# Kernel tuning notes

Hardware: AMD Instinct MI355X
Metric: run time of the kernel (lower is better)

Reference implementation:

```python
import jax, jax.numpy as jnp
import numpy as np

D_MODEL = 1024
N_HEAD = 16
HEAD_DIM = D_MODEL // N_HEAD
N_POS = 4096
K_PROJ = 256  # self.k is hardcoded to 256 in the module
BATCH = 4


def setup_inputs() -> dict:
    key = jax.random.key(0)
    ks = jax.random.split(key, 11)
    s = 1.0 / np.sqrt(D_MODEL)
    return {
        "x": jax.random.normal(ks[0], (BATCH, N_POS, D_MODEL), jnp.float32),
        "Wq": jax.random.normal(ks[1], (D_MODEL, D_MODEL), jnp.float32) * s,
        "bq": jnp.zeros((D_MODEL,), jnp.float32),
        "Wk": jax.random.normal(ks[2], (D_MODEL, D_MODEL), jnp.float32) * s,
        "bk": jnp.zeros((D_MODEL,), jnp.float32),
        "Wv": jax.random.normal(ks[3], (D_MODEL, D_MODEL), jnp.float32) * s,
        "bv": jnp.zeros((D_MODEL,), jnp.float32),
        "E": jax.random.normal(ks[4], (K_PROJ, N_POS), jnp.float32),
        "F": jax.random.normal(ks[5], (K_PROJ, N_POS), jnp.float32),
        "Wo": jax.random.normal(ks[6], (D_MODEL, D_MODEL), jnp.float32) * s,
        "bo": jnp.zeros((D_MODEL,), jnp.float32),
    }


def reference(x, Wq, bq, Wk, bk, Wv, bv, E, F, Wo, bo):
    B, N, D = x.shape
    scale = jnp.sqrt(jnp.asarray(HEAD_DIM, x.dtype))
    # Q/K/V projections (nn.Linear applies x @ W.T + b)
    def proj(W, b):
        y = jnp.einsum('bnd,ed->bne', x, W) + b
        return y.reshape(B, N, N_HEAD, HEAD_DIM).transpose(0, 2, 1, 3)  # bhnd
    Q = proj(Wq, bq)
    K = proj(Wk, bk)
    V = proj(Wv, bv)
    # Linformer low-rank projections along sequence dim
    Kp = jnp.einsum('kn,bhnd->bhkd', E, K)
    Vp = jnp.einsum('kn,bhnd->bhkd', F, V)
    attn_score = jnp.einsum('bhnd,bhkd->bhnk', Q, Kp) / scale
    attn = jax.nn.softmax(attn_score, axis=-1)  # dropout is identity (drop_prob=0)
    out = jnp.einsum('bhnk,bhkd->bhnd', attn, Vp)
    out = out.transpose(0, 2, 1, 3).reshape(B, N, D)
    out = jnp.einsum('bnd,ed->bne', out, Wo) + bo
    return out, attn_score
```

## Files before the change

kernel.cpp:

```cpp
#include <hip/hip_runtime.h>

typedef _Float16 f16;
typedef __attribute__((ext_vector_type(8))) _Float16 f16x8;
typedef __attribute__((ext_vector_type(4))) _Float16 f16x4;
typedef __attribute__((ext_vector_type(4))) float f32x4;

typedef const __attribute__((address_space(1))) unsigned int* gas_ptr;
typedef __attribute__((address_space(3))) unsigned int* las_ptr;

__device__ __forceinline__ void gload16(const f16* g, f16* l) {
  __builtin_amdgcn_global_load_lds((gas_ptr)g, (las_ptr)l, 16, 0, 0);
}

template<int WM, int WN, bool OUT32>
__device__ __forceinline__ void gemm_core(
    const f16* __restrict__ A, int lda,
    const f16* __restrict__ B, int ldb,
    int kLen,
    f16* lsA, f16* lsB,
    float* __restrict__ C32, f16* __restrict__ C16, int ldc,
    float scale, const float* __restrict__ biasC, const float* __restrict__ biasR)
{
  constexpr int T   = WM * WN * 64;
  constexpr int nA  = (WM * 64 * 8) / T;
  constexpr int nB  = (WN * 64 * 8) / T;
  constexpr int RPI = T / 8;
  const int t    = threadIdx.x;
  const int lane = t & 63;
  const int wave = t >> 6;
  const int wm   = wave / WN;
  const int wn   = wave % WN;

  f32x4 acc[4][4];
  const f32x4 z4 = {0.f, 0.f, 0.f, 0.f};
#pragma unroll
  for (int i = 0; i < 4; ++i)
#pragma unroll
    for (int j = 0; j < 4; ++j) acc[i][j] = z4;

  const int r_ = t >> 3;
  const int c_ = (t & 7) * 8;
  const int ldsOff = (wave << 9);

  for (int kt = 0; kt < kLen; kt += 64) {
#pragma unroll
    for (int i = 0; i < nA; ++i) {
      const f16* g = A + (size_t)(i * RPI + r_) * lda + kt + c_;
      gload16(g, lsA + i * (T * 8) + ldsOff);
    }
#pragma unroll
    for (int i = 0; i < nB; ++i) {
      const f16* g = B + (size_t)(i * RPI + r_) * ldb + kt + c_;
      gload16(g, lsB + i * (T * 8) + ldsOff);
    }
    __syncthreads();
#pragma unroll
    for (int ks = 0; ks < 2; ++ks) {
      f16x8 af[4], bf[4];
#pragma unroll
      for (int i = 0; i < 4; ++i)
        af[i] = *(const f16x8*)&lsA[(wm * 64 + i * 16 + (lane & 15)) * 64 + ks * 32 + (lane >> 4) * 8];
#pragma unroll
      for (int j = 0; j < 4; ++j)
        bf[j] = *(const f16x8*)&lsB[(wn * 64 + j * 16 + (lane & 15)) * 64 + ks * 32 + (lane >> 4) * 8];
#pragma unroll
      for (int i = 0; i < 4; ++i)
#pragma unroll
        for (int j = 0; j < 4; ++j)
          acc[i][j] = __builtin_amdgcn_mfma_f32_16x16x32_f16(af[i], bf[j], acc[i][j], 0, 0, 0);
    }
    __syncthreads();
  }

  const int lc = lane & 15;
  const int lr = (lane >> 4) * 4;
#pragma unroll
  for (int j = 0; j < 4; ++j) {
    const int col = wn * 64 + j * 16 + lc;
    const float bC = biasC ? biasC[col] : 0.f;
#pragma unroll
    for (int i = 0; i < 4; ++i) {
      const int rbase = wm * 64 + i * 16 + lr;
#pragma unroll
      for (int r = 0; r < 4; ++r) {
        const int row = rbase + r;
        float v = acc[i][j][r] * scale + bC;
        if (biasR) v += biasR[row];
        if (OUT32) C32[(size_t)row * ldc + col] = v;
        else       C16[(size_t)row * ldc + col] = (f16)v;
      }
    }
  }
}

template<int WM, int WN, bool OUT32>
__global__ __launch_bounds__(WM * WN * 64) void k_gemm(
    const f16* A, int lda, const f16* B, int ldb, int kLen,
    float* C32, f16* C16, int ldc, float scale,
    const float* biasC, const float* biasR)
{
  __shared__ f16 lsA[WM * 64 * 64];
  __shared__ f16 lsB[WN * 64 * 64];
  const size_t rt = blockIdx.y, ct = blockIdx.x;
  gemm_core<WM, WN, OUT32>(
      A + rt * (WM * 64) * (size_t)lda, lda,
      B + ct * (WN * 64) * (size_t)ldb, ldb, kLen,
      lsA, lsB,
      OUT32 ? C32 + rt * (WM * 64) * (size_t)ldc + ct * (WN * 64) : nullptr,
      OUT32 ? nullptr : C16 + rt * (WM * 64) * (size_t)ldc + ct * (WN * 64), ldc,
      scale,
      biasC ? biasC + ct * (WN * 64) : nullptr,
      biasR ? biasR + rt * (WM * 64) : nullptr);
}

__global__ __launch_bounds__(256) void k_cast_xt(const float* __restrict__ x,
                                                 f16* __restrict__ Xf,
                                                 f16* __restrict__ XT)
{
  __shared__ f16 tile[64][68];
  const int b = blockIdx.z, bi = blockIdx.y, bj = blockIdx.x;
  const int r0 = threadIdx.x >> 4;
  const int c4 = (threadIdx.x & 15) * 4;
  const float* xb = x + ((size_t)b * 4096 + (size_t)bi * 64) * 1024 + bj * 64;
#pragma unroll
  for (int rr = 0; rr < 4; ++rr) {
    const int row = rr * 16 + r0;
    const float4 v = *(const float4*)(xb + (size_t)row * 1024 + c4);
    f16x4 h = {(f16)v.x, (f16)v.y, (f16)v.z, (f16)v.w};
    *(f16x4*)&tile[row][c4] = h;
    *(f16x4*)(Xf + ((size_t)b * 4096 + (size_t)bi * 64 + row) * 1024 + bj * 64 + c4) = h;
  }
  __syncthreads();
#pragma unroll
  for (int rr = 0; rr < 4; ++rr) {
    const int col = rr * 16 + r0;
    f16x4 h = {tile[c4 + 0][col], tile[c4 + 1][col], tile[c4 + 2][col], tile[c4 + 3][col]};
    *(f16x4*)(XT + ((size_t)b * 1024 + (size_t)bj * 64 + col) * 4096 + (size_t)bi * 64 + c4) = h;
  }
}

__global__ __launch_bounds__(256) void k_cast_w(
    const float* w0, const float* w1, const float* w2,
    const float* w3, const float* w4, const float* w5, f16* __restrict__ d)
{
  const size_t i = ((size_t)blockIdx.x * 256 + threadIdx.x) * 4;
  const int seg = (int)(i >> 20);
  const float* s = (seg == 0) ? w0 : (seg == 1) ? w1 : (seg == 2) ? w2
                 : (seg == 3) ? w3 : (seg == 4) ? w4 : w5;
  const float4 v = *(const float4*)(s + (i & 1048575));
  f16x4 o = {(f16)v.x, (f16)v.y, (f16)v.z, (f16)v.w};
  *(f16x4*)(d + i) = o;
}

__global__ __launch_bounds__(256) void k_rowsum(const float* __restrict__ E,
                                                const float* __restrict__ F,
                                                float* __restrict__ rs)
{
  const int r = blockIdx.x * 4 + (threadIdx.x >> 6);
  const int lane = threadIdx.x & 63;
  const float* src = (r < 256) ? (E + (size_t)r * 4096) : (F + (size_t)(r - 256) * 4096);
  float s = 0.f;
#pragma unroll
  for (int i = 0; i < 16; ++i) {
    const float4 v = *(const float4*)(src + i * 256 + lane * 4);
    s += v.x + v.y + v.z + v.w;
  }
#pragma unroll
  for (int o = 32; o; o >>= 1) s += __shfl_xor(s, o);
  if (lane == 0) rs[r] = s;
}

__global__ __launch_bounds__(256) void k_exfx(const f16* __restrict__ EF,
                                              const f16* __restrict__ XT,
                                              float* __restrict__ part)
{
  __shared__ f16 lsA[128 * 64];
  __shared__ f16 lsB[128 * 64];
  const int z = blockIdx.z; const int b = z & 3; const int s = z >> 2;
  const int rt = blockIdx.y, ct = blockIdx.x;
  const f16* A = EF + (size_t)rt * 128 * 4096 + s * 1024;
  const f16* B = XT + (size_t)b * 1024 * 4096 + (size_t)ct * 128 * 4096 + s * 1024;
  float* C = part + (size_t)z * (512 * 1024) + (size_t)rt * 128 * 1024 + ct * 128;
  gemm_core<2, 2, true>(A, 4096, B, 4096, 1024, lsA, lsB, C, nullptr, 1024, 1.f, nullptr, nullptr);
}

__global__ __launch_bounds__(256) void k_reduce2(const float* __restrict__ part,
                                                 f16* __restrict__ EXf)
{
  const size_t i = ((size_t)blockIdx.x * 256 + threadIdx.x) * 4;
  const size_t b = i >> 19;
  const size_t idx = i & 524287;
  const float4 a = *(const float4*)(part + (0 * 4 + b) * 524288 + idx);
  const float4 c1 = *(const float4*)(part + (1 * 4 + b) * 524288 + idx);
  const float4 c2 = *(const float4*)(part + (2 * 4 + b) * 524288 + idx);
  const float4 c3 = *(const float4*)(part + (3 * 4 + b) * 524288 + idx);
  f16x4 o = {(f16)(a.x + c1.x + c2.x + c3.x), (f16)(a.y + c1.y + c2.y + c3.y),
             (f16)(a.z + c1.z + c2.z + c3.z), (f16)(a.w + c1.w + c2.w + c3.w)};
  *(f16x4*)(EXf + i) = o;
}

__global__ __launch_bounds__(256) void k_kpvp(const f16* __restrict__ EXf,
                                              const f16* __restrict__ W16,
                                              float* __restrict__ p2)
{
  __shared__ f16 lsA[128 * 64];
  __shared__ f16 lsB[128 * 64];
  const int z = blockIdx.z; const int which = z & 1; const int s = z >> 1;
  const int rt = blockIdx.y, ct = blockIdx.x;
  const f16 *A, *B;
  if (which == 0) {
    const int b = rt >> 1, r0 = (rt & 1) * 128;
    A = EXf + ((size_t)b * 512 + r0) * 1024 + s * 512;
    B = W16 + 1048576 + (size_t)ct * 128 * 1024 + s * 512;
  } else {
    const int b = ct >> 1, r0 = (ct & 1) * 128;
    A = W16 + 2 * 1048576 + (size_t)rt * 128 * 1024 + s * 512;
    B = EXf + ((size_t)b * 512 + 256 + r0) * 1024 + s * 512;
  }
  float* C = p2 + (size_t)(s * 2 + which) * 1048576 + (size_t)rt * 128 * 1024 + ct * 128;
  gemm_core<2, 2, true>(A, 1024, B, 1024, 512, lsA, lsB, C, nullptr, 1024, 1.f, nullptr, nullptr);
}

__global__ __launch_bounds__(256) void k_reduce3(const float* __restrict__ p2,
                                                 f16* __restrict__ KpVp,
                                                 const float* __restrict__ rs,
                                                 const float* __restrict__ bk,
                                                 const float* __restrict__ bv)
{
  const size_t i = ((size_t)blockIdx.x * 256 + threadIdx.x) * 4;
  const int half = (int)(i >> 20);
  const size_t j = i & 1048575;
  size_t pidx; float r1[4];
  if (half == 0) {
    const int r  = (int)((j >> 10) & 255);
    const int hd = (int)(j & 1023);
    pidx = j;
    const float se = rs[r];
#pragma unroll
    for (int t = 0; t < 4; ++t) r1[t] = se * bk[hd + t];
  } else {
    const int b  = (int)(j >> 18);
    const int hd = (int)((j >> 8) & 1023);
    const int r  = (int)(j & 255);
    pidx = (size_t)hd * 1024 + (size_t)b * 256 + r;
    const float bb = bv[hd];
#pragma unroll
    for (int t = 0; t < 4; ++t) r1[t] = bb * rs[256 + r + t];
  }
  const float4 a = *(const float4*)(p2 + (size_t)(0 * 2 + half) * 1048576 + pidx);
  const float4 c = *(const float4*)(p2 + (size_t)(1 * 2 + half) * 1048576 + pidx);
  f16x4 o = {(f16)(a.x + c.x + r1[0]), (f16)(a.y + c.y + r1[1]),
             (f16)(a.z + c.z + r1[2]), (f16)(a.w + c.w + r1[3])};
  *(f16x4*)(KpVp + i) = o;
}

__global__ __launch_bounds__(256) void k_scores(const f16* __restrict__ Q,
                                                const f16* __restrict__ Kp,
                                                float* __restrict__ S)
{
  __shared__ f16 lsA[128 * 64];
  __shared__ f16 lsB[128 * 64];
  const int bh = blockIdx.z; const int b = bh >> 4; const int h = bh & 15;
  const size_t rt = blockIdx.y, ct = blockIdx.x;
  const f16* A = Q + (size_t)b * 4096 * 1024 + h * 64 + rt * 128 * 1024;
  const f16* B = Kp + (size_t)b * 262144 + h * 64 + ct * 128 * 1024;
  float* C = S + (size_t)bh * 4096 * 256 + rt * 128 * 256 + ct * 128;
  gemm_core<2, 2, true>(A, 1024, B, 1024, 64, lsA, lsB, C, nullptr, 256, 0.125f, nullptr, nullptr);
}

__global__ __launch_bounds__(256) void k_pvsm(const float* __restrict__ S,
                                              const f16* __restrict__ VpT,
                                              f16* __restrict__ OP)
{
  __shared__ f16 lsP[128 * 256];
  __shared__ f16 lsV[64 * 256];
  const int rt = blockIdx.x, h = blockIdx.y, b = blockIdx.z;
  const int t = threadIdx.x, lane = t & 63, w = t >> 6;

  const char* Vb = (const char*)(VpT + ((size_t)b * 1024 + h * 64) * 256);
  {
    const int vrow = lane >> 5;
    const int voff = (lane & 31) * 16;
#pragma unroll
    for (int i = 0; i < 8; ++i) {
      const int row = i * 8 + w * 2 + vrow;
      const int so = voff ^ ((row & 7) << 4);
      gload16((const f16*)(Vb + (size_t)row * 512 + so),
              (f16*)((char*)lsV + i * 4096 + w * 1024));
    }
  }

  const float* Sb = S + (((size_t)(b * 16 + h)) * 4096 + (size_t)rt * 128) * 256;
  const int rg = t >> 4;
  const int li = t & 15;
#pragma unroll
  for (int it = 0; it < 8; ++it) {
    const int row = it * 16 + rg;
    const float* sr = Sb + (size_t)row * 256 + li * 16;
    const float4 v0 = *(const float4*)(sr + 0);
    const float4 v1 = *(const float4*)(sr + 4);
    const float4 v2 = *(const float4*)(sr + 8);
    const float4 v3 = *(const float4*)(sr + 12);
    float m = fmaxf(fmaxf(fmaxf(v0.x, v0.y), fmaxf(v0.z, v0.w)),
                    fmaxf(fmaxf(v1.x, v1.y), fmaxf(v1.z, v1.w)));
    m = fmaxf(m, fmaxf(fmaxf(fmaxf(v2.x, v2.y), fmaxf(v2.z, v2.w)),
                       fmaxf(fmaxf(v3.x, v3.y), fmaxf(v3.z, v3.w))));
#pragma unroll
    for (int o = 8; o; o >>= 1) m = fmaxf(m, __shfl_xor(m, o));
    float ev[16];
    ev[0]  = __expf(v0.x - m); ev[1]  = __expf(v0.y - m);
    ev[2]  = __expf(v0.z - m); ev[3]  = __expf(v0.w - m);
    ev[4]  = __expf(v1.x - m); ev[5]  = __expf(v1.y - m);
    ev[6]  = __expf(v1.z - m); ev[7]  = __expf(v1.w - m);
    ev[8]  = __expf(v2.x - m); ev[9]  = __expf(v2.y - m);
    ev[10] = __expf(v2.z - m); ev[11] = __expf(v2.w - m);
    ev[12] = __expf(v3.x - m); ev[13] = __expf(v3.y - m);
    ev[14] = __expf(v3.z - m); ev[15] = __expf(v3.w - m);
    float s = 0.f;
#pragma unroll
    for (int k2 = 0; k2 < 16; ++k2) s += ev[k2];
#pragma unroll
    for (int o = 8; o; o >>= 1) s += __shfl_xor(s, o);
    const float inv = 1.f / s;
    f16x8 h0, h1;
#pragma unroll
    for (int k2 = 0; k2 < 8; ++k2) {
      h0[k2] = (f16)(ev[k2] * inv);
      h1[k2] = (f16)(ev[8 + k2] * inv);
    }
    char* base = (char*)lsP + (size_t)row * 512;
    const int swz = (row & 7) << 4;
    *(f16x8*)(base + ((li * 32) ^ swz))      = h0;
    *(f16x8*)(base + ((li * 32 + 16) ^ swz)) = h1;
  }
  __syncthreads();

  const int wm = w >> 1, wn = w & 1;
  f32x4 acc[4][2];
  const f32x4 z4 = {0.f, 0.f, 0.f, 0.f};
#pragma unroll
  for (int i = 0; i < 4; ++i) { acc[i][0] = z4; acc[i][1] = z4; }
#pragma unroll
  for (int ks = 0; ks < 8; ++ks) {
    const int koff = ks * 64 + (lane >> 4) * 16;
    f16x8 af[4], bf[2];
#pragma unroll
    for (int i = 0; i < 4; ++i) {
      const int m = wm * 64 + i * 16 + (lane & 15);
      af[i] = *(const f16x8*)((const char*)lsP + (size_t)m * 512 + (koff ^ ((m & 7) << 4)));
    }
#pragma unroll
    for (int j = 0; j < 2; ++j) {
      const int n = wn * 32 + j * 16 + (lane & 15);
      bf[j] = *(const f16x8*)((const char*)lsV + (size_t)n * 512 + (koff ^ ((n & 7) << 4)));
    }
#pragma unroll
    for (int i = 0; i < 4; ++i)
#pragma unroll
      for (int j = 0; j < 2; ++j)
        acc[i][j] = __builtin_amdgcn_mfma_f32_16x16x32_f16(af[i], bf[j], acc[i][j], 0, 0, 0);
  }

  f16* Ob = OP + ((size_t)b * 4096 + (size_t)rt * 128) * 1024 + h * 64;
  const int lc = lane & 15, lr = (lane >> 4) * 4;
#pragma unroll
  for (int j = 0; j < 2; ++j) {
    const int col = wn * 32 + j * 16 + lc;
#pragma unroll
    for (int i = 0; i < 4; ++i) {
      const int rbase = wm * 64 + i * 16 + lr;
#pragma unroll
      for (int r = 0; r < 4; ++r)
        Ob[(size_t)(rbase + r) * 1024 + col] = (f16)acc[i][j][r];
    }
  }
}

extern "C" void kernel_launch(void* const* d_in, const int* in_sizes, int n_in,
                              void* d_out, int out_size, void* d_ws, size_t ws_size,
                              hipStream_t stream) {
  const float* x  = (const float*)d_in[0];
  const float* Wq = (const float*)d_in[1];
  const float* bq = (const float*)d_in[2];
  const float* Wk = (const float*)d_in[3];
  const float* bk = (const float*)d_in[4];
  const float* Wv = (const float*)d_in[5];
  const float* bv = (const float*)d_in[6];
  const float* E  = (const float*)d_in[7];
  const float* F  = (const float*)d_in[8];
  const float* Wo = (const float*)d_in[9];
  const float* bo = (const float*)d_in[10];

  float* out = (float*)d_out;
  float* S   = out + 16777216;

  char* w = (char*)d_ws;
  f16*   Xf     = (f16*)w;
  f16*   EXf    = (f16*)w;
  float* rowsum = (float*)(w + 4 * 1048576);
  f16*   XT     = (f16*)(w + 33554432);
  f16*   OPf    = (f16*)(w + 33554432);
  f16*   Qf     = (f16*)(w + (size_t)2 * 33554432);
  float* part   = (float*)(w + (size_t)3 * 33554432);
  float* part2  = (float*)(w + (size_t)3 * 33554432);
  f16*   W16    = (f16*)(w + (size_t)4 * 33554432);
  f16*   EF16   = W16 + (size_t)4 * 1048576;
  f16*   KpVp   = (f16*)(w + (size_t)4 * 33554432 + 12582912);

  k_cast_xt<<<dim3(16, 64, 4), 256, 0, stream>>>(x, Xf, XT);
  k_cast_w<<<6144, 256, 0, stream>>>(Wq, Wk, Wv, Wo, E, F, W16);

  k_gemm<2, 2, false><<<dim3(8, 128), 256, 0, stream>>>(
      Xf, 1024, W16, 1024, 1024, nullptr, Qf, 1024, 1.f, bq, nullptr);

  k_rowsum<<<128, 256, 0, stream>>>(E, F, rowsum);

  k_exfx<<<dim3(8, 4, 16), 256, 0, stream>>>(EF16, XT, part);
  k_reduce2<<<2048, 256, 0, stream>>>(part, EXf);

  k_kpvp<<<dim3(8, 8, 4), 256, 0, stream>>>(EXf, W16, part2);
  k_reduce3<<<2048, 256, 0, stream>>>(part2, KpVp, rowsum, bk, bv);

  k_scores<<<dim3(2, 32, 64), 256, 0, stream>>>(Qf, KpVp, S);

  k_pvsm<<<dim3(32, 16, 4), 256, 0, stream>>>(S, KpVp + (size_t)4 * 262144, OPf);

  k_gemm<2, 2, true><<<dim3(8, 128), 256, 0, stream>>>(
      OPf, 1024, W16 + 3 * 1048576, 1024, 1024, out, nullptr, 1024, 1.f, bo, nullptr);
}
```

Measured before the change: 724.4 us.

## Fuse score GEMM, softmax and PV GEMM into a single attention kernel

Merges the separate scores kernel and the softmax+PV kernel into one kernel. Each block computes Q·Kp^T for 128 rows in registers, writes the scaled scores to S (still a required output), runs the softmax on the register tiles and stages fp16 probabilities in LDS for the PV MFMA. This removes the global re-read of the 64 MB fp32 score tensor and one kernel launch. In exchange it uses 96 KB of shared memory and large accumulator arrays per thread, which may lower occupancy.

Measured after the change: 654.2 us. 9.7% less time.

```diff
diff --git a/kernel.cpp b/kernel.cpp
--- a/kernel.cpp
+++ b/kernel.cpp
@@ -254,31 +254,36 @@
   *(f16x4*)(KpVp + i) = o;
 }
 
-__global__ __launch_bounds__(256) void k_scores(const f16* __restrict__ Q,
-                                                const f16* __restrict__ Kp,
-                                                float* __restrict__ S)
-{
-  __shared__ f16 lsA[128 * 64];
-  __shared__ f16 lsB[128 * 64];
-  const int bh = blockIdx.z; const int b = bh >> 4; const int h = bh & 15;
-  const size_t rt = blockIdx.y, ct = blockIdx.x;
-  const f16* A = Q + (size_t)b * 4096 * 1024 + h * 64 + rt * 128 * 1024;
-  const f16* B = Kp + (size_t)b * 262144 + h * 64 + ct * 128 * 1024;
-  float* C = S + (size_t)bh * 4096 * 256 + rt * 128 * 256 + ct * 128;
-  gemm_core<2, 2, true>(A, 1024, B, 1024, 64, lsA, lsB, C, nullptr, 256, 0.125f, nullptr, nullptr);
-}
-
-__global__ __launch_bounds__(256) void k_pvsm(const float* __restrict__ S,
+__global__ __launch_bounds__(256) void k_attn(const f16* __restrict__ Q,
+                                              const f16* __restrict__ Kp,
                                               const f16* __restrict__ VpT,
+                                              float* __restrict__ S,
                                               f16* __restrict__ OP)
 {
-  __shared__ f16 lsP[128 * 256];
-  __shared__ f16 lsV[64 * 256];
+  __shared__ char smem[98304];
+  f16* lsK = (f16*)smem;
+  f16* lsQ = (f16*)(smem + 32768);
+  f16* lsV = (f16*)(smem + 65536);
+
   const int rt = blockIdx.x, h = blockIdx.y, b = blockIdx.z;
   const int t = threadIdx.x, lane = t & 63, w = t >> 6;
-
-  const char* Vb = (const char*)(VpT + ((size_t)b * 1024 + h * 64) * 256);
+  const int g = lane >> 4;
+  const int c = lane & 15;
+
+  const int r_ = t >> 3;
+  const int cswz = ((t & 7) * 16) ^ ((r_ & 7) << 4);
+  const char* Kg = (const char*)(Kp + (size_t)b * 262144 + h * 64);
+  const char* Qg = (const char*)(Q + ((size_t)b * 4096 + (size_t)rt * 128) * 1024 + h * 64);
+#pragma unroll
+  for (int i = 0; i < 8; ++i)
+    gload16((const f16*)(Kg + (size_t)(i * 32 + r_) * 2048 + cswz),
+            lsK + i * 2048 + (w << 9));
+#pragma unroll
+  for (int i = 0; i < 4; ++i)
+    gload16((const f16*)(Qg + (size_t)(i * 32 + r_) * 2048 + cswz),
+            lsQ + i * 2048 + (w << 9));
   {
+    const char* Vb = (const char*)(VpT + ((size_t)b * 1024 + h * 64) * 256);
     const int vrow = lane >> 5;
     const int voff = (lane & 31) * 16;
 #pragma unroll
@@ -289,89 +294,110 @@
               (f16*)((char*)lsV + i * 4096 + w * 1024));
     }
   }
-
-  const float* Sb = S + (((size_t)(b * 16 + h)) * 4096 + (size_t)rt * 128) * 256;
-  const int rg = t >> 4;
-  const int li = t & 15;
-#pragma unroll
-  for (int it = 0; it < 8; ++it) {
-    const int row = it * 16 + rg;
-    const float* sr = Sb + (size_t)row * 256 + li * 16;
-    const float4 v0 = *(const float4*)(sr + 0);
-    const float4 v1 = *(const float4*)(sr + 4);
-    const float4 v2 = *(const float4*)(sr + 8);
-    const float4 v3 = *(const float4*)(sr + 12);
-    float m = fmaxf(fmaxf(fmaxf(v0.x, v0.y), fmaxf(v0.z, v0.w)),
-                    fmaxf(fmaxf(v1.x, v1.y), fmaxf(v1.z, v1.w)));
-    m = fmaxf(m, fmaxf(fmaxf(fmaxf(v2.x, v2.y), fmaxf(v2.z, v2.w)),
-                       fmaxf(fmaxf(v3.x, v3.y), fmaxf(v3.z, v3.w))));
-#pragma unroll
-    for (int o = 8; o; o >>= 1) m = fmaxf(m, __shfl_xor(m, o));
-    float ev[16];
-    ev[0]  = __expf(v0.x - m); ev[1]  = __expf(v0.y - m);
-    ev[2]  = __expf(v0.z - m); ev[3]  = __expf(v0.w - m);
-    ev[4]  = __expf(v1.x - m); ev[5]  = __expf(v1.y - m);
-    ev[6]  = __expf(v1.z - m); ev[7]  = __expf(v1.w - m);
-    ev[8]  = __expf(v2.x - m); ev[9]  = __expf(v2.y - m);
-    ev[10] = __expf(v2.z - m); ev[11] = __expf(v2.w - m);
-    ev[12] = __expf(v3.x - m); ev[13] = __expf(v3.y - m);
-    ev[14] = __expf(v3.z - m); ev[15] = __expf(v3.w - m);
+  __syncthreads();
+
+  const int swz = (lane & 7) << 4;
+  f32x4 acc[16][2];
+  const f32x4 z4 = {0.f, 0.f, 0.f, 0.f};
+#pragma unroll
+  for (int i = 0; i < 16; ++i) { acc[i][0] = z4; acc[i][1] = z4; }
+#pragma unroll
+  for (int ks = 0; ks < 2; ++ks) {
+    const int koff = ks * 64 + g * 16;
+    f16x8 bf[2];
+#pragma unroll
+    for (int j = 0; j < 2; ++j) {
+      const int row = w * 32 + j * 16 + c;
+      bf[j] = *(const f16x8*)((const char*)lsQ + row * 128 + (koff ^ swz));
+    }
+#pragma unroll
+    for (int i = 0; i < 16; ++i) {
+      const f16x8 af = *(const f16x8*)((const char*)lsK + (i * 16 + c) * 128 + (koff ^ swz));
+      acc[i][0] = __builtin_amdgcn_mfma_f32_16x16x32_f16(af, bf[0], acc[i][0], 0, 0, 0);
+      acc[i][1] = __builtin_amdgcn_mfma_f32_16x16x32_f16(af, bf[1], acc[i][1], 0, 0, 0);
+    }
+  }
+
+  float* Sb = S + (((size_t)(b * 16 + h)) * 4096 + (size_t)rt * 128 + w * 32) * 256;
+#pragma unroll
+  for (int j = 0; j < 2; ++j)
+#pragma unroll
+    for (int i = 0; i < 16; ++i) {
+      acc[i][j] *= 0.125f;
+      *(f32x4*)(Sb + (size_t)(j * 16 + c) * 256 + i * 16 + g * 4) = acc[i][j];
+    }
+
+  float pinv[2];
+#pragma unroll
+  for (int j = 0; j < 2; ++j) {
+    float m = acc[0][j][0];
+#pragma unroll
+    for (int i = 0; i < 16; ++i)
+      m = fmaxf(m, fmaxf(fmaxf(acc[i][j][0], acc[i][j][1]),
+                         fmaxf(acc[i][j][2], acc[i][j][3])));
+    m = fmaxf(m, __shfl_xor(m, 16));
+    m = fmaxf(m, __shfl_xor(m, 32));
     float s = 0.f;
 #pragma unroll
-    for (int k2 = 0; k2 < 16; ++k2) s += ev[k2];
-#pragma unroll
-    for (int o = 8; o; o >>= 1) s += __shfl_xor(s, o);
-    const float inv = 1.f / s;
-    f16x8 h0, h1;
-#pragma unroll
-    for (int k2 = 0; k2 < 8; ++k2) {
-      h0[k2] = (f16)(ev[k2] * inv);
-      h1[k2] = (f16)(ev[8 + k2] * inv);
-    }
-    char* base = (char*)lsP + (size_t)row * 512;
-    const int swz = (row & 7) << 4;
-    *(f16x8*)(base + ((li * 32) ^ swz))      = h0;
-    *(f16x8*)(base + ((li * 32 + 16) ^ swz)) = h1;
-  }
+    for (int i = 0; i < 16; ++i)
+#pragma unroll
+      for (int r2 = 0; r2 < 4; ++r2) {
+        const float e = __expf(acc[i][j][r2] - m);
+        acc[i][j][r2] = e;
+        s += e;
+      }
+    s += __shfl_xor(s, 16);
+    s += __shfl_xor(s, 32);
+    pinv[j] = 1.f / s;
+  }
+
   __syncthreads();
-
-  const int wm = w >> 1, wn = w & 1;
-  f32x4 acc[4][2];
-  const f32x4 z4 = {0.f, 0.f, 0.f, 0.f};
-#pragma unroll
-  for (int i = 0; i < 4; ++i) { acc[i][0] = z4; acc[i][1] = z4; }
+  char* lsP = (char*)smem;
+#pragma unroll
+  for (int j = 0; j < 2; ++j) {
+    const int n = w * 32 + j * 16 + c;
+    char* base = lsP + n * 512;
+#pragma unroll
+    for (int i = 0; i < 16; ++i) {
+      f16x4 p = {(f16)(acc[i][j][0] * pinv[j]), (f16)(acc[i][j][1] * pinv[j]),
+                 (f16)(acc[i][j][2] * pinv[j]), (f16)(acc[i][j][3] * pinv[j])};
+      *(f16x4*)(base + ((i * 32 + g * 8) ^ swz)) = p;
+    }
+  }
+  __syncthreads();
+
+  f32x4 o[2][4];
+#pragma unroll
+  for (int i2 = 0; i2 < 2; ++i2)
+#pragma unroll
+    for (int jh = 0; jh < 4; ++jh) o[i2][jh] = z4;
 #pragma unroll
   for (int ks = 0; ks < 8; ++ks) {
-    const int koff = ks * 64 + (lane >> 4) * 16;
-    f16x8 af[4], bf[2];
-#pragma unroll
-    for (int i = 0; i < 4; ++i) {
-      const int m = wm * 64 + i * 16 + (lane & 15);
-      af[i] = *(const f16x8*)((const char*)lsP + (size_t)m * 512 + (koff ^ ((m & 7) << 4)));
-    }
-#pragma unroll
-    for (int j = 0; j < 2; ++j) {
-      const int n = wn * 32 + j * 16 + (lane & 15);
-      bf[j] = *(const f16x8*)((const char*)lsV + (size_t)n * 512 + (koff ^ ((n & 7) << 4)));
-    }
-#pragma unroll
-    for (int i = 0; i < 4; ++i)
-#pragma unroll
-      for (int j = 0; j < 2; ++j)
-        acc[i][j] = __builtin_amdgcn_mfma_f32_16x16x32_f16(af[i], bf[j], acc[i][j], 0, 0, 0);
-  }
-
-  f16* Ob = OP + ((size_t)b * 4096 + (size_t)rt * 128) * 1024 + h * 64;
-  const int lc = lane & 15, lr = (lane >> 4) * 4;
-#pragma unroll
-  for (int j = 0; j < 2; ++j) {
-    const int col = wn * 32 + j * 16 + lc;
-#pragma unroll
-    for (int i = 0; i < 4; ++i) {
-      const int rbase = wm * 64 + i * 16 + lr;
-#pragma unroll
-      for (int r = 0; r < 4; ++r)
-        Ob[(size_t)(rbase + r) * 1024 + col] = (f16)acc[i][j][r];
+    const int koff = ks * 64 + g * 16;
+    f16x8 pa[2];
+#pragma unroll
+    for (int i2 = 0; i2 < 2; ++i2) {
+      const int n = w * 32 + i2 * 16 + c;
+      pa[i2] = *(const f16x8*)(lsP + n * 512 + (koff ^ swz));
+    }
+#pragma unroll
+    for (int jh = 0; jh < 4; ++jh) {
+      const f16x8 vb = *(const f16x8*)((const char*)lsV + (jh * 16 + c) * 512 + (koff ^ swz));
+      o[0][jh] = __builtin_amdgcn_mfma_f32_16x16x32_f16(pa[0], vb, o[0][jh], 0, 0, 0);
+      o[1][jh] = __builtin_amdgcn_mfma_f32_16x16x32_f16(pa[1], vb, o[1][jh], 0, 0, 0);
+    }
+  }
+
+  f16* Ob = OP + ((size_t)b * 4096 + (size_t)rt * 128 + w * 32) * 1024 + h * 64;
+#pragma unroll
+  for (int jh = 0; jh < 4; ++jh) {
+    const int col = jh * 16 + c;
+#pragma unroll
+    for (int i2 = 0; i2 < 2; ++i2) {
+      const int rb = i2 * 16 + g * 4;
+#pragma unroll
+      for (int r2 = 0; r2 < 4; ++r2)
+        Ob[(size_t)(rb + r2) * 1024 + col] = (f16)o[i2][jh][r2];
     }
   }
 }
@@ -421,9 +447,8 @@
   k_kpvp<<<dim3(8, 8, 4), 256, 0, stream>>>(EXf, W16, part2);
   k_reduce3<<<2048, 256, 0, stream>>>(part2, KpVp, rowsum, bk, bv);
 
-  k_scores<<<dim3(2, 32, 64), 256, 0, stream>>>(Qf, KpVp, S);
-
-  k_pvsm<<<dim3(32, 16, 4), 256, 0, stream>>>(S, KpVp + (size_t)4 * 262144, OPf);
+  k_attn<<<dim3(32, 16, 4), 256, 0, stream>>>(
+      Qf, KpVp, KpVp + (size_t)4 * 262144, S, OPf);
 
   k_gemm<2, 2, true><<<dim3(8, 128), 256, 0, stream>>>(
       OPf, 1024, W16 + 3 * 1048576, 1024, 1024, out, nullptr, 1024, 1.f, bo, nullptr);
```
